# Kernel tuning notes

Hardware: AMD Instinct MI355X
Metric: run time of the kernel (lower is better)

Reference implementation:

```python
import jax, jax.numpy as jnp
import numpy as np

N_RES = 8192
N_IN = 256
B = 16
NNZ_RES = int(0.1 * N_RES * N_RES)  # 6,710,886
NNZ_IN = int(0.1 * N_RES * N_IN)    # 209,715
RES_SCALE = 0.9
IN_SCALE = 0.4
BIAS_SCALE = 0.1
A_LEAK = 1.0  # leaky_erf default


def setup_inputs() -> dict:
    key = jax.random.key(0)
    ks = jax.random.split(key, 9)
    state = jax.random.normal(ks[0], (B, N_RES), jnp.float32)
    x = jax.random.normal(ks[1], (B, N_IN), jnp.float32)
    res_vals = RES_SCALE * jax.random.normal(ks[2], (NNZ_RES,), jnp.float32)
    res_rows = jax.random.randint(ks[3], (NNZ_RES,), 0, N_RES, jnp.int32)
    res_cols = jax.random.randint(ks[4], (NNZ_RES,), 0, N_RES, jnp.int32)
    res_bias = BIAS_SCALE * jax.random.normal(ks[5], (N_RES,), jnp.float32)
    in_vals = IN_SCALE * jax.random.normal(ks[6], (NNZ_IN,), jnp.float32)
    in_rows = jax.random.randint(ks[7], (NNZ_IN,), 0, N_RES, jnp.int32)
    in_cols = jax.random.randint(ks[8], (NNZ_IN,), 0, N_IN, jnp.int32)
    return {"state": state, "x": x,
            "res_vals": res_vals, "res_rows": res_rows, "res_cols": res_cols,
            "res_bias": res_bias,
            "in_vals": in_vals, "in_rows": in_rows, "in_cols": in_cols}


def _coo_matmat_T(vals, rows, cols, X, n_out):
    """Computes (A @ X.T).T where A is COO [n_out, n_in], X is [B, n_in].

    out[b, r] = sum_k vals[k] * X[b, cols[k]] for rows[k] == r.
    Mirrors sparse_ops.coo_matmat(vals, rows, cols, X.T).T in the flax module.
    """
    data = vals[:, None] * jnp.take(X.T, cols, axis=0)  # [nnz, B]
    out = jax.ops.segment_sum(data, rows, num_segments=n_out)  # [n_out, B]
    return out.T  # [B, n_out]


def reference(state, x, res_vals, res_rows, res_cols, res_bias, in_vals, in_rows, in_cols):
    z_input = _coo_matmat_T(in_vals, in_rows, in_cols, x, N_RES)       # [B, N_RES]
    z_res = _coo_matmat_T(res_vals, res_rows, res_cols, state, N_RES)  # [B, N_RES]
    z = z_input + z_res + res_bias
    # leaky_erf(z, prev_state, a) = (1 - a) * prev_state + a * erf(z)
    return (1.0 - A_LEAK) * state + A_LEAK * jax.lax.erf(z)
```

## Files before the change

kernel.cpp:

```cpp
#include <hip/hip_runtime.h>
#include <math.h>

#define N_RES 8192
#define N_IN  256
#define BATCH 16

__global__ void init_kernel(const float* __restrict__ state,
                            const float* __restrict__ x,
                            const float* __restrict__ bias,
                            float* __restrict__ z_acc,
                            float* __restrict__ state_T,
                            float* __restrict__ x_T) {
    int i = blockIdx.x * blockDim.x + threadIdx.x;
    if (i < N_RES * BATCH) {
        int r = i >> 4;
        int b = i & 15;
        state_T[i] = state[b * N_RES + r];
        z_acc[i]   = bias[r];
    }
    if (i < N_IN * BATCH) {
        int c = i >> 4;
        int b = i & 15;
        x_T[i] = x[b * N_IN + c];
    }
}

__global__ void scatter_kernel(const float* __restrict__ vals,
                               const int* __restrict__ rows,
                               const int* __restrict__ cols,
                               const float* __restrict__ src_T,
                               float* __restrict__ z_acc,
                               int nnz) {
    int tid = blockIdx.x * blockDim.x + threadIdx.x;
    int g   = tid >> 4;
    int b   = tid & 15;
    int ngroups = (gridDim.x * blockDim.x) >> 4;
    for (int k = g; k < nnz; k += ngroups) {
        float v = vals[k];
        int   r = rows[k];
        int   c = cols[k];
        float s = src_T[(c << 4) + b];
        unsafeAtomicAdd(&z_acc[(r << 4) + b], v * s);
    }
}

__global__ void finish_kernel(const float* __restrict__ z_acc,
                              float* __restrict__ out) {
    int i = blockIdx.x * blockDim.x + threadIdx.x;
    if (i < N_RES * BATCH) {
        int b = i >> 13;
        int r = i & (N_RES - 1);
        out[i] = erff(z_acc[(r << 4) + b]);
    }
}

extern "C" void kernel_launch(void* const* d_in, const int* in_sizes, int n_in,
                              void* d_out, int out_size, void* d_ws, size_t ws_size,
                              hipStream_t stream) {
    const float* state    = (const float*)d_in[0];
    const float* x        = (const float*)d_in[1];
    const float* res_vals = (const float*)d_in[2];
    const int*   res_rows = (const int*)  d_in[3];
    const int*   res_cols = (const int*)  d_in[4];
    const float* res_bias = (const float*)d_in[5];
    const float* in_vals  = (const float*)d_in[6];
    const int*   in_rows  = (const int*)  d_in[7];
    const int*   in_cols  = (const int*)  d_in[8];
    float* out = (float*)d_out;

    float* ws      = (float*)d_ws;
    float* z_acc   = ws;
    float* state_T = z_acc + N_RES * BATCH;
    float* x_T     = state_T + N_RES * BATCH;

    int nnz_res = in_sizes[2];
    int nnz_in  = in_sizes[6];

    init_kernel<<<(N_RES * BATCH + 255) / 256, 256, 0, stream>>>(
        state, x, res_bias, z_acc, state_T, x_T);

    scatter_kernel<<<2048, 256, 0, stream>>>(
        res_vals, res_rows, res_cols, state_T, z_acc, nnz_res);

    scatter_kernel<<<512, 256, 0, stream>>>(
        in_vals, in_rows, in_cols, x_T, z_acc, nnz_in);

    finish_kernel<<<(N_RES * BATCH + 255) / 256, 256, 0, stream>>>(z_acc, out);
}
```

Measured before the change: 462.7 us.

## Privatize sparse accumulation into LDS per row range and fuse both products

Replaces the two global-atomic scatter kernels with one fused kernel. Each block takes a slice of the nonzeros and one of four output row ranges, and accumulates into a 2048x16 shared-memory tile using LDS atomics. It then flushes the tile to global memory with rotated atomic adds. This removes most of the contended global atomics. In exchange, every block rereads its whole nonzero slice four times, skipping rows outside its range, and the large LDS footprint leaves room for only one block per CU.

```diff
diff --git a/kernel.cpp b/kernel.cpp
--- a/kernel.cpp
+++ b/kernel.cpp
@@ -1,9 +1,14 @@
 #include <hip/hip_runtime.h>
 #include <math.h>
 
-#define N_RES 8192
-#define N_IN  256
-#define BATCH 16
+#define N_RES  8192
+#define N_IN   256
+#define BATCH  16
+#define NRANGE 4
+#define RROWS  2048
+#define CHUNK  2048
+#define NSLICE 64
+#define TPB    512
 
 __global__ void init_kernel(const float* __restrict__ state,
                             const float* __restrict__ x,
@@ -25,22 +30,102 @@
     }
 }
 
-__global__ void scatter_kernel(const float* __restrict__ vals,
-                               const int* __restrict__ rows,
-                               const int* __restrict__ cols,
-                               const float* __restrict__ src_T,
-                               float* __restrict__ z_acc,
-                               int nnz) {
-    int tid = blockIdx.x * blockDim.x + threadIdx.x;
-    int g   = tid >> 4;
-    int b   = tid & 15;
-    int ngroups = (gridDim.x * blockDim.x) >> 4;
-    for (int k = g; k < nnz; k += ngroups) {
-        float v = vals[k];
-        int   r = rows[k];
-        int   c = cols[k];
-        float s = src_T[(c << 4) + b];
-        unsafeAtomicAdd(&z_acc[(r << 4) + b], v * s);
+__global__ __launch_bounds__(TPB)
+void accum_kernel(const float* __restrict__ res_vals,
+                  const int*   __restrict__ res_rows,
+                  const int*   __restrict__ res_cols,
+                  const float* __restrict__ in_vals,
+                  const int*   __restrict__ in_rows,
+                  const int*   __restrict__ in_cols,
+                  const float* __restrict__ state_T,
+                  const float* __restrict__ x_T,
+                  float* __restrict__ z_acc,
+                  int nnz_res, int nnz_in) {
+    __shared__ float zl[RROWS * BATCH];
+    __shared__ __align__(16) float sv[CHUNK];
+    __shared__ __align__(16) int   sr[CHUNK];
+    __shared__ __align__(16) int   sc[CHUNK];
+
+    const int bid   = blockIdx.x;
+    const int slice = bid >> 2;
+    const int range = bid & (NRANGE - 1);
+    const int rbase = range * RROWS;
+    const int tid   = threadIdx.x;
+    const int g     = tid >> 4;
+    const int lane  = tid & 15;
+
+    for (int i = tid; i < RROWS * BATCH; i += TPB) zl[i] = 0.0f;
+
+    {
+        int chunks_total = (nnz_res + CHUNK - 1) / CHUNK;
+        int cps = (chunks_total + NSLICE - 1) / NSLICE;
+        int s_begin = slice * cps * CHUNK;
+        int s_end   = s_begin + cps * CHUNK;
+        if (s_end > nnz_res) s_end = nnz_res;
+        for (int chunk = s_begin; chunk < s_end; chunk += CHUNK) {
+            int cnt = s_end - chunk; if (cnt > CHUNK) cnt = CHUNK;
+            __syncthreads();
+            if (cnt == CHUNK) {
+                int i4 = tid << 2;
+                *(float4*)&sv[i4] = *(const float4*)&res_vals[chunk + i4];
+                *(int4*)  &sr[i4] = *(const int4*)  &res_rows[chunk + i4];
+                *(int4*)  &sc[i4] = *(const int4*)  &res_cols[chunk + i4];
+            } else {
+                for (int i = tid; i < cnt; i += TPB) {
+                    sv[i] = res_vals[chunk + i];
+                    sr[i] = res_rows[chunk + i];
+                    sc[i] = res_cols[chunk + i];
+                }
+            }
+            __syncthreads();
+            for (int i = g; i < cnt; i += 32) {
+                unsigned d = (unsigned)(sr[i] - rbase);
+                if (d < RROWS) {
+                    float s = state_T[(sc[i] << 4) + lane];
+                    atomicAdd(&zl[(d << 4) + lane], sv[i] * s);
+                }
+            }
+        }
+    }
+
+    {
+        int chunks_total = (nnz_in + CHUNK - 1) / CHUNK;
+        int cps = (chunks_total + NSLICE - 1) / NSLICE;
+        int s_begin = slice * cps * CHUNK;
+        int s_end   = s_begin + cps * CHUNK;
+        if (s_end > nnz_in) s_end = nnz_in;
+        for (int chunk = s_begin; chunk < s_end; chunk += CHUNK) {
+            int cnt = s_end - chunk; if (cnt > CHUNK) cnt = CHUNK;
+            __syncthreads();
+            if (cnt == CHUNK) {
+                int i4 = tid << 2;
+                *(float4*)&sv[i4] = *(const float4*)&in_vals[chunk + i4];
+                *(int4*)  &sr[i4] = *(const int4*)  &in_rows[chunk + i4];
+                *(int4*)  &sc[i4] = *(const int4*)  &in_cols[chunk + i4];
+            } else {
+                for (int i = tid; i < cnt; i += TPB) {
+                    sv[i] = in_vals[chunk + i];
+                    sr[i] = in_rows[chunk + i];
+                    sc[i] = in_cols[chunk + i];
+                }
+            }
+            __syncthreads();
+            for (int i = g; i < cnt; i += 32) {
+                unsigned d = (unsigned)(sr[i] - rbase);
+                if (d < RROWS) {
+                    float s = x_T[(sc[i] << 4) + lane];
+                    atomicAdd(&zl[(d << 4) + lane], sv[i] * s);
+                }
+            }
+        }
+    }
+
+    __syncthreads();
+
+    int rot = (slice * 32) & (RROWS - 1);
+    for (int k = 0; k < RROWS / 32; ++k) {
+        int r = (g + k * 32 + rot) & (RROWS - 1);
+        unsafeAtomicAdd(&z_acc[((rbase + r) << 4) + lane], zl[(r << 4) + lane]);
     }
 }
 
@@ -79,11 +164,9 @@
     init_kernel<<<(N_RES * BATCH + 255) / 256, 256, 0, stream>>>(
         state, x, res_bias, z_acc, state_T, x_T);
 
-    scatter_kernel<<<2048, 256, 0, stream>>>(
-        res_vals, res_rows, res_cols, state_T, z_acc, nnz_res);
-
-    scatter_kernel<<<512, 256, 0, stream>>>(
-        in_vals, in_rows, in_cols, x_T, z_acc, nnz_in);
+    accum_kernel<<<NSLICE * NRANGE, TPB, 0, stream>>>(
+        res_vals, res_rows, res_cols, in_vals, in_rows, in_cols,
+        state_T, x_T, z_acc, nnz_res, nnz_in);
 
     finish_kernel<<<(N_RES * BATCH + 255) / 256, 256, 0, stream>>>(z_acc, out);
 }
```

Result: slower. 1.062 ms (+129.6%).

## Bin nonzeros by row range and accumulate in shared memory

Applied to the files above, without the earlier changes.

Adds a binning pass that partitions combined reservoir and input nonzeros into 16 row-range buckets, packing value plus row/col/source flag into a float2. A second kernel assigns blocks to row ranges and slices, accumulating into a 512x16 shared-memory tile with LDS atomics before flushing to global with fewer global atomics. This trades random global atomics for an extra read/write pass over the nonzeros. It relies on a large workspace and a fixed per-bucket capacity, and silently drops entries beyond that capacity.

```diff
diff --git a/kernel.cpp b/kernel.cpp
--- a/kernel.cpp
+++ b/kernel.cpp
@@ -4,13 +4,24 @@
 #define N_RES 8192
 #define N_IN  256
 #define BATCH 16
+
+#define NRANGE  16
+#define RROWS   512
+#define CAP     475136
+#define P1_TPB  256
+#define P1_ITER 8
+#define P1_TILE (P1_TPB * P1_ITER)
+#define P1_GRID 1024
+#define NSLICE2 32
+#define P2_TPB  512
 
 __global__ void init_kernel(const float* __restrict__ state,
                             const float* __restrict__ x,
                             const float* __restrict__ bias,
                             float* __restrict__ z_acc,
                             float* __restrict__ state_T,
-                            float* __restrict__ x_T) {
+                            float* __restrict__ x_T,
+                            int* __restrict__ gcount) {
     int i = blockIdx.x * blockDim.x + threadIdx.x;
     if (i < N_RES * BATCH) {
         int r = i >> 4;
@@ -22,6 +33,138 @@
         int c = i >> 4;
         int b = i & 15;
         x_T[i] = x[b * N_IN + c];
+    }
+    if (i < NRANGE) gcount[i] = 0;
+}
+
+__global__ __launch_bounds__(P1_TPB)
+void bin_kernel(const float* __restrict__ res_vals,
+                const int*   __restrict__ res_rows,
+                const int*   __restrict__ res_cols,
+                const float* __restrict__ in_vals,
+                const int*   __restrict__ in_rows,
+                const int*   __restrict__ in_cols,
+                float2* __restrict__ bucket,
+                int*    __restrict__ gcount,
+                int nnz_res, int nnz_total) {
+    __shared__ int hcount[NRANGE];
+    __shared__ int hbase[NRANGE];
+    __shared__ int gbase[NRANGE];
+    __shared__ float2 stage[P1_TILE];
+
+    const int tid = threadIdx.x;
+    const int ntiles = (nnz_total + P1_TILE - 1) / P1_TILE;
+
+    for (int tile = blockIdx.x; tile < ntiles; tile += gridDim.x) {
+        const int base = tile * P1_TILE;
+        if (tid < NRANGE) hcount[tid] = 0;
+        __syncthreads();
+
+        float    ev[P1_ITER];
+        unsigned ep[P1_ITER];
+        int      erg[P1_ITER];
+        int      eslot[P1_ITER];
+        #pragma unroll
+        for (int j = 0; j < P1_ITER; ++j) {
+            int idx = base + j * P1_TPB + tid;
+            erg[j] = -1;
+            if (idx < nnz_total) {
+                float v; int r, c; unsigned flag;
+                if (idx < nnz_res) {
+                    v = res_vals[idx]; r = res_rows[idx]; c = res_cols[idx]; flag = 0u;
+                } else {
+                    int k = idx - nnz_res;
+                    v = in_vals[k]; r = in_rows[k]; c = in_cols[k]; flag = 1u << 22;
+                }
+                int rg = r >> 9;
+                unsigned d = (unsigned)(r & (RROWS - 1));
+                ev[j] = v;
+                ep[j] = flag | (d << 13) | (unsigned)c;
+                erg[j] = rg;
+                eslot[j] = atomicAdd(&hcount[rg], 1);
+            }
+        }
+        __syncthreads();
+        if (tid < NRANGE) gbase[tid] = atomicAdd(&gcount[tid], hcount[tid]);
+        if (tid == 0) {
+            int s = 0;
+            #pragma unroll
+            for (int r = 0; r < NRANGE; ++r) { hbase[r] = s; s += hcount[r]; }
+        }
+        __syncthreads();
+        #pragma unroll
+        for (int j = 0; j < P1_ITER; ++j)
+            if (erg[j] >= 0)
+                stage[hbase[erg[j]] + eslot[j]] = make_float2(ev[j], __uint_as_float(ep[j]));
+        __syncthreads();
+
+        const int tot = hbase[NRANGE - 1] + hcount[NRANGE - 1];
+        for (int k = tid; k < tot; k += P1_TPB) {
+            int lo = 0;
+            #pragma unroll
+            for (int step = 8; step >= 1; step >>= 1) {
+                int cand = lo + step;
+                if (cand < NRANGE && hbase[cand] <= k) lo = cand;
+            }
+            int go = gbase[lo] + (k - hbase[lo]);
+            if (go < CAP) bucket[(size_t)lo * CAP + go] = stage[k];
+        }
+    }
+}
+
+__device__ __forceinline__ void process_entry(float2 e, int lane,
+                                              const float* __restrict__ state_T,
+                                              const float* __restrict__ x_T,
+                                              float* __restrict__ zl) {
+    unsigned u = __float_as_uint(e.y);
+    const float* sp = (u & (1u << 22)) ? x_T : state_T;
+    float s = sp[(int)((u & 0x1FFFu) << 4) + lane];
+    atomicAdd(&zl[(int)(((u >> 13) & 0x1FFu) << 4) + lane], e.x * s);
+}
+
+__global__ __launch_bounds__(P2_TPB)
+void accum2_kernel(const float2* __restrict__ bucket,
+                   const int*    __restrict__ gcount,
+                   const float*  __restrict__ state_T,
+                   const float*  __restrict__ x_T,
+                   float* __restrict__ z_acc) {
+    __shared__ float zl[RROWS * BATCH];
+    const int tid   = threadIdx.x;
+    const int range = (int)blockIdx.x >> 5;
+    const int slice = (int)blockIdx.x & (NSLICE2 - 1);
+    const int g     = tid >> 4;
+    const int lane  = tid & 15;
+
+    for (int i = tid; i < RROWS * BATCH; i += P2_TPB) zl[i] = 0.0f;
+    __syncthreads();
+
+    int cnt = gcount[range]; if (cnt > CAP) cnt = CAP;
+    int per = (cnt + NSLICE2 - 1) / NSLICE2;
+    int start = slice * per;
+    int end = start + per; if (end > cnt) end = cnt;
+
+    const float2* bk = bucket + (size_t)range * CAP;
+    int k = start + g;
+    for (; k + 96 < end; k += 128) {
+        float2 e0 = bk[k];
+        float2 e1 = bk[k + 32];
+        float2 e2 = bk[k + 64];
+        float2 e3 = bk[k + 96];
+        process_entry(e0, lane, state_T, x_T, zl);
+        process_entry(e1, lane, state_T, x_T, zl);
+        process_entry(e2, lane, state_T, x_T, zl);
+        process_entry(e3, lane, state_T, x_T, zl);
+    }
+    for (; k < end; k += 32) process_entry(bk[k], lane, state_T, x_T, zl);
+
+    __syncthreads();
+
+    const int rot = (slice * 16) & (RROWS - 1);
+    const int rbase = range * RROWS;
+    #pragma unroll
+    for (int kk = 0; kk < RROWS / 32; ++kk) {
+        int r = (g + kk * 32 + rot) & (RROWS - 1);
+        unsafeAtomicAdd(&z_acc[((rbase + r) << 4) + lane], zl[(r << 4) + lane]);
     }
 }
 
@@ -72,18 +215,30 @@
     float* z_acc   = ws;
     float* state_T = z_acc + N_RES * BATCH;
     float* x_T     = state_T + N_RES * BATCH;
+    int*   gcount  = (int*)(x_T + N_IN * BATCH);
+    float2* bucket = (float2*)(gcount + 16);
+
+    const size_t required = (size_t)(N_RES * BATCH * 2 + N_IN * BATCH + 16) * 4
+                          + (size_t)NRANGE * CAP * sizeof(float2);
 
     int nnz_res = in_sizes[2];
     int nnz_in  = in_sizes[6];
 
     init_kernel<<<(N_RES * BATCH + 255) / 256, 256, 0, stream>>>(
-        state, x, res_bias, z_acc, state_T, x_T);
-
-    scatter_kernel<<<2048, 256, 0, stream>>>(
-        res_vals, res_rows, res_cols, state_T, z_acc, nnz_res);
-
-    scatter_kernel<<<512, 256, 0, stream>>>(
-        in_vals, in_rows, in_cols, x_T, z_acc, nnz_in);
+        state, x, res_bias, z_acc, state_T, x_T, gcount);
+
+    if (ws_size >= required) {
+        bin_kernel<<<P1_GRID, P1_TPB, 0, stream>>>(
+            res_vals, res_rows, res_cols, in_vals, in_rows, in_cols,
+            bucket, gcount, nnz_res, nnz_res + nnz_in);
+        accum2_kernel<<<NRANGE * NSLICE2, P2_TPB, 0, stream>>>(
+            bucket, gcount, state_T, x_T, z_acc);
+    } else {
+        scatter_kernel<<<2048, 256, 0, stream>>>(
+            res_vals, res_rows, res_cols, state_T, z_acc, nnz_res);
+        scatter_kernel<<<512, 256, 0, stream>>>(
+            in_vals, in_rows, in_cols, x_T, z_acc, nnz_in);
+    }
 
     finish_kernel<<<(N_RES * BATCH + 255) / 256, 256, 0, stream>>>(z_acc, out);
 }
```

After: 715.8 us. +54.7%, slower.

## Bin COO entries into 2D row/column tiles and accumulate in LDS

Applied to the files above, without the earlier changes.

Adds a binning pass that sorts nonzeros into 512x512 row/column tile buckets, packing the value and local indices into a float2. Per-tile blocks then stage the source slice in LDS and accumulate with LDS atomics before flushing to global with one atomic per output element. The aim is to replace millions of scattered global atomics and gathers with on-chip work. In exchange it needs a large workspace, falls back to the old path when the workspace is too small, and silently drops entries past each bucket's fixed capacity.

```diff
diff --git a/kernel.cpp b/kernel.cpp
--- a/kernel.cpp
+++ b/kernel.cpp
@@ -4,13 +4,35 @@
 #define N_RES 8192
 #define N_IN  256
 #define BATCH 16
+
+#define NCR       16
+#define NRR       16
+#define NBKT_MAIN 256
+#define NBKT      272
+#define CAP_M     28672
+#define CAP_I     16128
+#define RR        512
+#define CC        512
+
+#define B2_TPB  512
+#define B2_ITER 8
+#define B2_TILE (B2_TPB * B2_ITER)
+
+#define A3_TPB 512
+#define NS     2
+
+__device__ __forceinline__ void lds_fadd(float* p, float v) {
+    unsigned a = (unsigned)(uintptr_t)p;
+    asm volatile("ds_add_f32 %0, %1" : : "v"(a), "v"(v));
+}
 
 __global__ void init_kernel(const float* __restrict__ state,
                             const float* __restrict__ x,
                             const float* __restrict__ bias,
                             float* __restrict__ z_acc,
                             float* __restrict__ state_T,
-                            float* __restrict__ x_T) {
+                            float* __restrict__ x_T,
+                            int* __restrict__ gcount) {
     int i = blockIdx.x * blockDim.x + threadIdx.x;
     if (i < N_RES * BATCH) {
         int r = i >> 4;
@@ -22,6 +44,208 @@
         int c = i >> 4;
         int b = i & 15;
         x_T[i] = x[b * N_IN + c];
+    }
+    if (i < 512) gcount[i] = 0;
+}
+
+__global__ __launch_bounds__(B2_TPB)
+void bin2d_kernel(const float* __restrict__ rv,
+                  const int*   __restrict__ rrow,
+                  const int*   __restrict__ rcol,
+                  const float* __restrict__ iv,
+                  const int*   __restrict__ irow,
+                  const int*   __restrict__ icol,
+                  float2* __restrict__ bucket,
+                  float2* __restrict__ in_bucket,
+                  int*    __restrict__ gcount,
+                  int nnz_res, int nnz_total) {
+    __shared__ int whist[8][NBKT];
+    __shared__ int tot[NBKT];
+    __shared__ int sc[NBKT];
+    __shared__ int gbase[NBKT];
+    __shared__ float2 stage[B2_TILE];
+
+    const int tid  = threadIdx.x;
+    const int wave = tid >> 6;
+    const int base = blockIdx.x * B2_TILE;
+
+    for (int i = tid; i < 8 * NBKT; i += B2_TPB) (&whist[0][0])[i] = 0;
+    __syncthreads();
+
+    float    ev[B2_ITER];
+    unsigned em[B2_ITER];
+    int      ebk[B2_ITER];
+    int      esl[B2_ITER];
+    #pragma unroll
+    for (int j = 0; j < B2_ITER; ++j) {
+        int idx = base + j * B2_TPB + tid;
+        ebk[j] = -1;
+        if (idx < nnz_total) {
+            float v; int r, c, bk; unsigned m;
+            if (idx < nnz_res) {
+                v = rv[idx]; r = rrow[idx]; c = rcol[idx];
+                bk = ((r >> 9) << 4) | (c >> 9);
+                m  = ((unsigned)(r & 511) << 9) | (unsigned)(c & 511);
+            } else {
+                int k2 = idx - nnz_res;
+                v = iv[k2]; r = irow[k2]; c = icol[k2];
+                bk = NBKT_MAIN + (r >> 9);
+                m  = ((unsigned)(r & 511) << 9) | (unsigned)c;
+            }
+            ev[j] = v; em[j] = m; ebk[j] = bk;
+            esl[j] = atomicAdd(&whist[wave][bk], 1);
+        }
+    }
+    __syncthreads();
+
+    if (tid < NBKT) {
+        int s = 0;
+        #pragma unroll
+        for (int w = 0; w < 8; ++w) { int t = whist[w][tid]; whist[w][tid] = s; s += t; }
+        tot[tid] = s; sc[tid] = s;
+    }
+    __syncthreads();
+    for (int off = 1; off < NBKT; off <<= 1) {
+        int v = 0;
+        if (tid < NBKT && tid >= off) v = sc[tid - off];
+        __syncthreads();
+        if (tid < NBKT) sc[tid] += v;
+        __syncthreads();
+    }
+    if (tid < NBKT) {
+        int t = tot[tid];
+        if (t > 0) gbase[tid] = atomicAdd(&gcount[tid], t);
+    }
+    __syncthreads();
+
+    #pragma unroll
+    for (int j = 0; j < B2_ITER; ++j)
+        if (ebk[j] >= 0) {
+            int bk = ebk[j];
+            int slot = (sc[bk] - tot[bk]) + whist[wave][bk] + esl[j];
+            stage[slot] = make_float2(ev[j], __uint_as_float(em[j]));
+        }
+    __syncthreads();
+
+    const int tot_all = sc[NBKT - 1];
+    for (int k = tid; k < tot_all; k += B2_TPB) {
+        int lo = 0;
+        #pragma unroll
+        for (int step = 256; step >= 1; step >>= 1) {
+            int cand = lo + step;
+            if (cand < NBKT && (sc[cand] - tot[cand]) <= k) lo = cand;
+        }
+        int off2 = k - (sc[lo] - tot[lo]);
+        int go = gbase[lo] + off2;
+        if (lo < NBKT_MAIN) {
+            if (go < CAP_M) bucket[(size_t)lo * CAP_M + go] = stage[k];
+        } else {
+            if (go < CAP_I) in_bucket[(size_t)(lo - NBKT_MAIN) * CAP_I + go] = stage[k];
+        }
+    }
+}
+
+__device__ __forceinline__ void proc_main(float2 e, int lane,
+                                          const float* __restrict__ ls,
+                                          float* __restrict__ zl) {
+    unsigned u = __float_as_uint(e.y);
+    float s = ls[(int)((u & 511u) << 4) + lane];
+    lds_fadd(&zl[(int)((u >> 9) << 4) + lane], e.x * s);
+}
+
+__global__ __launch_bounds__(A3_TPB)
+void accum3_kernel(const float2* __restrict__ bucket,
+                   const int*    __restrict__ gcount,
+                   const float*  __restrict__ state_T,
+                   float* __restrict__ z_acc) {
+    __shared__ float ls[CC * BATCH];
+    __shared__ float zl[RR * BATCH];
+    const int tid   = threadIdx.x;
+    const int bkt   = (int)blockIdx.x >> 1;
+    const int slice = (int)blockIdx.x & (NS - 1);
+    const int rrng  = bkt >> 4;
+    const int crng  = bkt & 15;
+    const int g     = tid >> 4;
+    const int lane  = tid & 15;
+
+    {
+        const float4* src = (const float4*)(state_T + ((crng * CC) << 4));
+        float4* dst = (float4*)ls;
+        #pragma unroll 4
+        for (int i = tid; i < CC * BATCH / 4; i += A3_TPB) dst[i] = src[i];
+    }
+    for (int i = tid; i < RR * BATCH; i += A3_TPB) zl[i] = 0.0f;
+    __syncthreads();
+
+    int cnt = gcount[bkt]; if (cnt > CAP_M) cnt = CAP_M;
+    int per = (cnt + NS - 1) / NS;
+    int start = slice * per;
+    int end = start + per; if (end > cnt) end = cnt;
+    const float2* bk = bucket + (size_t)bkt * CAP_M;
+
+    int k = start + g;
+    for (; k + 96 < end; k += 128) {
+        float2 e0 = bk[k];
+        float2 e1 = bk[k + 32];
+        float2 e2 = bk[k + 64];
+        float2 e3 = bk[k + 96];
+        proc_main(e0, lane, ls, zl);
+        proc_main(e1, lane, ls, zl);
+        proc_main(e2, lane, ls, zl);
+        proc_main(e3, lane, ls, zl);
+    }
+    for (; k < end; k += 32) proc_main(bk[k], lane, ls, zl);
+
+    asm volatile("s_waitcnt lgkmcnt(0)");
+    __syncthreads();
+
+    const int rbase = rrng * RR;
+    const int rot = (crng * 32 + slice * 16) & (RR - 1);
+    #pragma unroll
+    for (int kk = 0; kk < RR / 32; ++kk) {
+        int r = (g + kk * 32 + rot) & (RR - 1);
+        unsafeAtomicAdd(&z_acc[((rbase + r) << 4) + lane], zl[(r << 4) + lane]);
+    }
+}
+
+__global__ __launch_bounds__(A3_TPB)
+void accum_in_kernel(const float2* __restrict__ in_bucket,
+                     const int*    __restrict__ gcount,
+                     const float*  __restrict__ x_T,
+                     float* __restrict__ z_acc) {
+    __shared__ float lx[N_IN * BATCH];
+    __shared__ float zl[RR * BATCH];
+    const int tid   = threadIdx.x;
+    const int bkt   = (int)blockIdx.x >> 1;
+    const int slice = (int)blockIdx.x & 1;
+    const int g     = tid >> 4;
+    const int lane  = tid & 15;
+
+    {
+        const float4* src = (const float4*)x_T;
+        float4* dst = (float4*)lx;
+        for (int i = tid; i < N_IN * BATCH / 4; i += A3_TPB) dst[i] = src[i];
+    }
+    for (int i = tid; i < RR * BATCH; i += A3_TPB) zl[i] = 0.0f;
+    __syncthreads();
+
+    int cnt = gcount[NBKT_MAIN + bkt]; if (cnt > CAP_I) cnt = CAP_I;
+    int per = (cnt + 1) / 2;
+    int start = slice * per;
+    int end = start + per; if (end > cnt) end = cnt;
+    const float2* bk = in_bucket + (size_t)bkt * CAP_I;
+
+    for (int k = start + g; k < end; k += 32) proc_main(bk[k], lane, lx, zl);
+
+    asm volatile("s_waitcnt lgkmcnt(0)");
+    __syncthreads();
+
+    const int rbase = bkt * RR;
+    const int rot = (slice * 256) & (RR - 1);
+    #pragma unroll
+    for (int kk = 0; kk < RR / 32; ++kk) {
+        int r = (g + kk * 32 + rot) & (RR - 1);
+        unsafeAtomicAdd(&z_acc[((rbase + r) << 4) + lane], zl[(r << 4) + lane]);
     }
 }
 
@@ -68,22 +292,40 @@
     const int*   in_cols  = (const int*)  d_in[8];
     float* out = (float*)d_out;
 
-    float* ws      = (float*)d_ws;
-    float* z_acc   = ws;
-    float* state_T = z_acc + N_RES * BATCH;
-    float* x_T     = state_T + N_RES * BATCH;
-
-    int nnz_res = in_sizes[2];
-    int nnz_in  = in_sizes[6];
+    float*  ws        = (float*)d_ws;
+    float*  z_acc     = ws;
+    float*  state_T   = z_acc + N_RES * BATCH;
+    float*  x_T       = state_T + N_RES * BATCH;
+    int*    gcount    = (int*)(x_T + N_IN * BATCH);
+    float2* bucket    = (float2*)(gcount + 512);
+    float2* in_bucket = bucket + (size_t)NBKT_MAIN * CAP_M;
+
+    const size_t required = (size_t)(N_RES * BATCH * 2 + N_IN * BATCH + 512) * 4
+                          + (size_t)NBKT_MAIN * CAP_M * sizeof(float2)
+                          + (size_t)16 * CAP_I * sizeof(float2);
+
+    int nnz_res   = in_sizes[2];
+    int nnz_in    = in_sizes[6];
+    int nnz_total = nnz_res + nnz_in;
 
     init_kernel<<<(N_RES * BATCH + 255) / 256, 256, 0, stream>>>(
-        state, x, res_bias, z_acc, state_T, x_T);
-
-    scatter_kernel<<<2048, 256, 0, stream>>>(
-        res_vals, res_rows, res_cols, state_T, z_acc, nnz_res);
-
-    scatter_kernel<<<512, 256, 0, stream>>>(
-        in_vals, in_rows, in_cols, x_T, z_acc, nnz_in);
+        state, x, res_bias, z_acc, state_T, x_T, gcount);
+
+    if (ws_size >= required) {
+        int tiles = (nnz_total + B2_TILE - 1) / B2_TILE;
+        bin2d_kernel<<<tiles, B2_TPB, 0, stream>>>(
+            res_vals, res_rows, res_cols, in_vals, in_rows, in_cols,
+            bucket, in_bucket, gcount, nnz_res, nnz_total);
+        accum3_kernel<<<NBKT_MAIN * NS, A3_TPB, 0, stream>>>(
+            bucket, gcount, state_T, z_acc);
+        accum_in_kernel<<<16 * 2, A3_TPB, 0, stream>>>(
+            in_bucket, gcount, x_T, z_acc);
+    } else {
+        scatter_kernel<<<2048, 256, 0, stream>>>(
+            res_vals, res_rows, res_cols, state_T, z_acc, nnz_res);
+        scatter_kernel<<<512, 256, 0, stream>>>(
+            in_vals, in_rows, in_cols, x_T, z_acc, nnz_in);
+    }
 
     finish_kernel<<<(N_RES * BATCH + 255) / 256, 256, 0, stream>>>(z_acc, out);
 }
```

Result: slower. 864.6 us (+86.9%).
